# Kernel optimization log

Measured on AMD Instinct MI355X. Metric: run time of the kernel, lower is better.

The kernel has to match this reference:

```python
import jax, jax.numpy as jnp
import numpy as np

B, S, D, H, O = 4, 128, 768, 768, 2

def setup_inputs() -> dict:
    key = jax.random.key(0)
    ks = jax.random.split(key, 6)
    scale = 1.0 / np.sqrt(2 * D)
    return {
        "a": jax.random.normal(ks[0], (B, S, D), jnp.float32),
        "b": jax.random.normal(ks[1], (B, S, D), jnp.float32),
        "W1": jax.random.normal(ks[2], (2 * D, H), jnp.float32) * scale,
        "b1": jax.random.normal(ks[3], (H,), jnp.float32) * 0.01,
        "W2": jax.random.normal(ks[4], (H, O), jnp.float32) * (1.0 / np.sqrt(H)),
        "b2": jax.random.normal(ks[5], (O,), jnp.float32) * 0.01,
    }

def reference(a, b, W1, b1, W2, b2):
    # Pairwise concat [a_i ; b_j] followed by Linear(2D->H) is algebraically
    # identical to projecting a and b separately and broadcast-adding
    # (biaffine-style rewrite; same math as cat+matmul, less HBM traffic).
    d = a.shape[-1]
    ha = jnp.einsum('bsd,dh->bsh', a, W1[:d])        # (B, Sa, H)
    hb = jnp.einsum('btd,dh->bth', b, W1[d:])        # (B, Sb, H)
    h = jax.nn.relu(ha[:, :, None, :] + hb[:, None, :, :] + b1)  # (B, Sa, Sb, H)
    scores = jnp.einsum('bsth,ho->bsto', h, W2) + b2  # (B, Sa, Sb, O)
    return scores
```

## Files before the change

### kernel.cpp

```cpp
#include <hip/hip_runtime.h>
#include <hip/hip_fp16.h>


typedef __attribute__((ext_vector_type(2))) _Float16 half2t;
typedef __attribute__((ext_vector_type(8))) _Float16 half8t;
typedef __attribute__((ext_vector_type(4))) float floatx4;
typedef unsigned int uint;

__device__ __forceinline__ half2t pkrtz(float x, float y) {
    __fp16 r __attribute__((ext_vector_type(2))) = __builtin_amdgcn_cvt_pkrtz(x, y);
    half2t o; __builtin_memcpy(&o, &r, 4); return o;
}

__global__ __launch_bounds__(256) void gemm_kernel(
    const float* __restrict__ a, const float* __restrict__ bmat,
    const float* __restrict__ W1, const float* __restrict__ b1,
    const float* __restrict__ W2,
    ushort* __restrict__ Hf,
    uint* __restrict__ W2pk)
{
    const int which = blockIdx.z;
    const int n0 = blockIdx.x * 32;
    const int m0 = blockIdx.y * 32;
    const int t  = threadIdx.x;

    if (blockIdx.x == 0 && blockIdx.y == 0 && which == 0) {
#pragma unroll
        for (int j = t; j < 768; j += 256) {
            const int o  = (j >= 384) ? 1 : 0;
            const int h2 = j - o * 384;
            half2t pw = pkrtz(W2[4 * h2 + o], W2[4 * h2 + 2 + o]);
            uint u; __builtin_memcpy(&u, &pw, 4);
            W2pk[j] = u;
        }
    }

    __shared__ ushort As[2][32][72];
    __shared__ ushort Bs[2][32][72];

    const int arow = t >> 3;
    const int akc  = (t & 7) * 8;
    const float* __restrict__ Asrc = which ? bmat : a;
    const float* __restrict__ aptr = Asrc + (size_t)(m0 + arow) * 768 + akc;

    const int ncol = t & 31;
    const int kg   = (t >> 5) * 8;
    const float* __restrict__ bptr = W1 + (size_t)(which * 768 + kg) * 768 + n0 + ncol;

    const int lane = t & 63;
    const int w    = t >> 6;
    const int mh   = w >> 1;
    const int nh   = w & 1;
    const int lr   = lane & 15;
    const int lq   = lane >> 4;

    floatx4 acc = {0, 0, 0, 0};

    float4 a4[2];
    float  br[8];
    a4[0] = *(const float4*)(aptr);
    a4[1] = *(const float4*)(aptr + 4);
#pragma unroll
    for (int j = 0; j < 8; j++) br[j] = bptr[(size_t)j * 768];

    int p = 0;
    for (int kt = 0; kt < 768; kt += 64, p ^= 1) {
        half2t ap[4];
        ap[0] = pkrtz(a4[0].x, a4[0].y);
        ap[1] = pkrtz(a4[0].z, a4[0].w);
        ap[2] = pkrtz(a4[1].x, a4[1].y);
        ap[3] = pkrtz(a4[1].z, a4[1].w);
        __builtin_memcpy(&As[p][arow][akc], ap, 16);
        half2t bp[4];
#pragma unroll
        for (int j = 0; j < 4; j++) bp[j] = pkrtz(br[2 * j], br[2 * j + 1]);
        __builtin_memcpy(&Bs[p][ncol][kg], bp, 16);

        __syncthreads();

        if (kt + 64 < 768) {
            a4[0] = *(const float4*)(aptr + kt + 64);
            a4[1] = *(const float4*)(aptr + kt + 68);
#pragma unroll
            for (int j = 0; j < 8; j++)
                br[j] = bptr[(size_t)(kt + 64 + j) * 768];
        }

#pragma unroll
        for (int h = 0; h < 2; h++) {
            const int kb = h * 32 + lq * 8;
            half8t afr, bfr;
            __builtin_memcpy(&afr, &As[p][mh * 16 + lr][kb], 16);
            __builtin_memcpy(&bfr, &Bs[p][nh * 16 + lr][kb], 16);
            acc = __builtin_amdgcn_mfma_f32_16x16x32_f16(afr, bfr, acc, 0, 0, 0);
        }
    }

    const int ncolO = n0 + nh * 16 + lr;
    const float bias = which ? 0.f : b1[ncolO];
    ushort* __restrict__ dst = Hf + (size_t)which * 393216 + ncolO;
    const int rbase = m0 + mh * 16 + lq * 4;
#pragma unroll
    for (int r = 0; r < 4; r++) {
        _Float16 v = (_Float16)(acc[r] + bias);
        ushort u; __builtin_memcpy(&u, &v, 2);
        dst[(size_t)(rbase + r) * 768] = u;
    }
}

__global__ __launch_bounds__(256) void pair_kernel(
    const ushort* __restrict__ Hf, const uint* __restrict__ W2pk,
    const float* __restrict__ b2, float* __restrict__ out)
{
    const int bb = blockIdx.z >> 1;
    const int hh = blockIdx.z & 1;
    const int s0 = blockIdx.y * 16;
    const int t0 = blockIdx.x * 16;
    const int tid = threadIdx.x;

    __shared__ ushort hAs[16][392];
    __shared__ ushort hBs[16][392];

    const int hbase = hh * 384;
    const ushort* __restrict__ Asrc = Hf +          (size_t)(bb * 128 + s0) * 768 + hbase;
    const ushort* __restrict__ Bsrc = Hf + 393216 + (size_t)(bb * 128 + t0) * 768 + hbase;

#pragma unroll
    for (int i = 0; i < 3; i++) {
        const int c   = tid + i * 256;
        const int row = c / 48;
        const int col = (c % 48) * 8;
        *(uint4*)&hAs[row][col] = *(const uint4*)(Asrc + (size_t)row * 768 + col);
        *(uint4*)&hBs[row][col] = *(const uint4*)(Bsrc + (size_t)row * 768 + col);
    }
    __syncthreads();

    const int sl = tid >> 4;
    const int tl = tid & 15;
    const ushort* __restrict__ arow = &hAs[sl][0];
    const ushort* __restrict__ brow = &hBs[tl][0];
    const uint* __restrict__ w2o0 = W2pk +       hh * 192;
    const uint* __restrict__ w2o1 = W2pk + 384 + hh * 192;

    float acc0 = 0.f, acc1 = 0.f;
    const half2t zero = {(_Float16)0.f, (_Float16)0.f};

#pragma unroll 8
    for (int h8 = 0; h8 < 384; h8 += 8) {
        half2t pa[4], pb[4], w0[4], w1[4];
        __builtin_memcpy(pa, arow + h8, 16);
        __builtin_memcpy(pb, brow + h8, 16);
        __builtin_memcpy(w0, &w2o0[h8 / 2], 16);
        __builtin_memcpy(w1, &w2o1[h8 / 2], 16);
#pragma unroll
        for (int j = 0; j < 4; j++) {
            half2t s = pa[j] + pb[j];
            s = __builtin_elementwise_max(s, zero);
            acc0 = __builtin_amdgcn_fdot2(s, w0[j], acc0, false);
            acc1 = __builtin_amdgcn_fdot2(s, w1[j], acc1, false);
        }
    }

    if (hh == 0) { acc0 += b2[0]; acc1 += b2[1]; }
    const int sg = bb * 128 + s0 + sl;
    const int tg = t0 + tl;
    float* ob = &out[((size_t)sg * 128 + tg) * 2];
    unsafeAtomicAdd(ob,     acc0);
    unsafeAtomicAdd(ob + 1, acc1);
}

extern "C" void kernel_launch(void* const* d_in, const int* in_sizes, int n_in,
                              void* d_out, int out_size, void* d_ws, size_t ws_size,
                              hipStream_t stream) {
    const float* a  = (const float*)d_in[0];
    const float* b  = (const float*)d_in[1];
    const float* W1 = (const float*)d_in[2];
    const float* b1 = (const float*)d_in[3];
    const float* W2 = (const float*)d_in[4];
    const float* b2 = (const float*)d_in[5];
    float* out = (float*)d_out;

    ushort* Hf   = (ushort*)d_ws;
    uint*   W2pk = (uint*)((char*)d_ws + (2 << 20));

    gemm_kernel<<<dim3(24, 16, 2), 256, 0, stream>>>(a, b, W1, b1, W2, Hf, W2pk);
    pair_kernel<<<dim3(8, 8, 8), 256, 0, stream>>>(Hf, W2pk, b2, out);
}
```

Baseline: 85.15 us.

## Register-block pair kernel 2x2 per thread and split hidden dim eight ways

Each pair_kernel thread now computes a 2x2 block of (s,t) pairs, so every loaded A row, B row and W2 value is reused across four pairs and LDS and register load traffic per output drops. The hidden dimension is split into eight 96-wide slices instead of two 384-wide halves, which keeps the grid at 512 blocks while each block covers a 32x32 tile. The cost is four times as many atomic adds into the output and more accumulator registers per thread.

```diff
diff --git a/kernel.cpp b/kernel.cpp
--- a/kernel.cpp
+++ b/kernel.cpp
@@ -10,6 +10,9 @@
 __device__ __forceinline__ half2t pkrtz(float x, float y) {
     __fp16 r __attribute__((ext_vector_type(2))) = __builtin_amdgcn_cvt_pkrtz(x, y);
     half2t o; __builtin_memcpy(&o, &r, 4); return o;
+}
+__device__ __forceinline__ half2t h2cast(uint u) {
+    half2t o; __builtin_memcpy(&o, &u, 4); return o;
 }
 
 __global__ __launch_bounds__(256) void gemm_kernel(
@@ -112,61 +115,90 @@
     const ushort* __restrict__ Hf, const uint* __restrict__ W2pk,
     const float* __restrict__ b2, float* __restrict__ out)
 {
-    const int bb = blockIdx.z >> 1;
-    const int hh = blockIdx.z & 1;
-    const int s0 = blockIdx.y * 16;
-    const int t0 = blockIdx.x * 16;
+    const int bb = blockIdx.z >> 3;
+    const int hh = blockIdx.z & 7;
+    const int s0 = blockIdx.y * 32;
+    const int t0 = blockIdx.x * 32;
     const int tid = threadIdx.x;
 
-    __shared__ ushort hAs[16][392];
-    __shared__ ushort hBs[16][392];
-
-    const int hbase = hh * 384;
+    __shared__ ushort hAs[32][104];
+    __shared__ ushort hBs[32][104];
+
+    const int hbase = hh * 96;
     const ushort* __restrict__ Asrc = Hf +          (size_t)(bb * 128 + s0) * 768 + hbase;
     const ushort* __restrict__ Bsrc = Hf + 393216 + (size_t)(bb * 128 + t0) * 768 + hbase;
 
 #pragma unroll
     for (int i = 0; i < 3; i++) {
         const int c   = tid + i * 256;
-        const int row = c / 48;
-        const int col = (c % 48) * 8;
-        *(uint4*)&hAs[row][col] = *(const uint4*)(Asrc + (size_t)row * 768 + col);
-        *(uint4*)&hBs[row][col] = *(const uint4*)(Bsrc + (size_t)row * 768 + col);
+        const int arr = c >= 384;
+        const int cc  = c - arr * 384;
+        const int row = cc / 12;
+        const int ch  = (cc % 12) * 8;
+        const ushort* src = arr ? Bsrc : Asrc;
+        ushort* dst = arr ? &hBs[row][ch] : &hAs[row][ch];
+        *(uint4*)dst = *(const uint4*)(src + (size_t)row * 768 + ch);
     }
     __syncthreads();
 
     const int sl = tid >> 4;
     const int tl = tid & 15;
-    const ushort* __restrict__ arow = &hAs[sl][0];
-    const ushort* __restrict__ brow = &hBs[tl][0];
-    const uint* __restrict__ w2o0 = W2pk +       hh * 192;
-    const uint* __restrict__ w2o1 = W2pk + 384 + hh * 192;
-
-    float acc0 = 0.f, acc1 = 0.f;
+    const ushort* __restrict__ arow0 = &hAs[2 * sl][0];
+    const ushort* __restrict__ arow1 = &hAs[2 * sl + 1][0];
+    const ushort* __restrict__ brow0 = &hBs[2 * tl][0];
+    const ushort* __restrict__ brow1 = &hBs[2 * tl + 1][0];
+    const uint* __restrict__ w2o0 = W2pk +       hh * 48;
+    const uint* __restrict__ w2o1 = W2pk + 384 + hh * 48;
+
+    float acc[2][2][2] = {};
     const half2t zero = {(_Float16)0.f, (_Float16)0.f};
 
-#pragma unroll 8
-    for (int h8 = 0; h8 < 384; h8 += 8) {
-        half2t pa[4], pb[4], w0[4], w1[4];
-        __builtin_memcpy(pa, arow + h8, 16);
-        __builtin_memcpy(pb, brow + h8, 16);
+#pragma unroll
+    for (int h8 = 0; h8 < 96; h8 += 8) {
+        uint pa0[4], pa1[4], pb0[4], pb1[4], w0[4], w1[4];
+        __builtin_memcpy(pa0, arow0 + h8, 16);
+        __builtin_memcpy(pa1, arow1 + h8, 16);
+        __builtin_memcpy(pb0, brow0 + h8, 16);
+        __builtin_memcpy(pb1, brow1 + h8, 16);
         __builtin_memcpy(w0, &w2o0[h8 / 2], 16);
         __builtin_memcpy(w1, &w2o1[h8 / 2], 16);
 #pragma unroll
-        for (int j = 0; j < 4; j++) {
-            half2t s = pa[j] + pb[j];
-            s = __builtin_elementwise_max(s, zero);
-            acc0 = __builtin_amdgcn_fdot2(s, w0[j], acc0, false);
-            acc1 = __builtin_amdgcn_fdot2(s, w1[j], acc1, false);
-        }
-    }
-
-    if (hh == 0) { acc0 += b2[0]; acc1 += b2[1]; }
-    const int sg = bb * 128 + s0 + sl;
-    const int tg = t0 + tl;
-    float* ob = &out[((size_t)sg * 128 + tg) * 2];
-    unsafeAtomicAdd(ob,     acc0);
-    unsafeAtomicAdd(ob + 1, acc1);
+        for (int d = 0; d < 4; d++) {
+            const half2t a0 = h2cast(pa0[d]), a1 = h2cast(pa1[d]);
+            const half2t b0 = h2cast(pb0[d]), b1 = h2cast(pb1[d]);
+            const half2t v0 = h2cast(w0[d]),  v1 = h2cast(w1[d]);
+            half2t s;
+            s = __builtin_elementwise_max(a0 + b0, zero);
+            acc[0][0][0] = __builtin_amdgcn_fdot2(s, v0, acc[0][0][0], false);
+            acc[0][0][1] = __builtin_amdgcn_fdot2(s, v1, acc[0][0][1], false);
+            s = __builtin_elementwise_max(a0 + b1, zero);
+            acc[0][1][0] = __builtin_amdgcn_fdot2(s, v0, acc[0][1][0], false);
+            acc[0][1][1] = __builtin_amdgcn_fdot2(s, v1, acc[0][1][1], false);
+            s = __builtin_elementwise_max(a1 + b0, zero);
+            acc[1][0][0] = __builtin_amdgcn_fdot2(s, v0, acc[1][0][0], false);
+            acc[1][0][1] = __builtin_amdgcn_fdot2(s, v1, acc[1][0][1], false);
+            s = __builtin_elementwise_max(a1 + b1, zero);
+            acc[1][1][0] = __builtin_amdgcn_fdot2(s, v0, acc[1][1][0], false);
+            acc[1][1][1] = __builtin_amdgcn_fdot2(s, v1, acc[1][1][1], false);
+        }
+    }
+
+    if (hh == 0) {
+#pragma unroll
+        for (int i = 0; i < 2; i++)
+#pragma unroll
+            for (int j = 0; j < 2; j++) {
+                acc[i][j][0] += b2[0];
+                acc[i][j][1] += b2[1];
+            }
+    }
+    const int sg = bb * 128 + s0 + 2 * sl;
+    const int tg = t0 + 2 * tl;
+    float* ob = &out[(size_t)sg * 256 + tg * 2];
+    unsafeAtomicAdd(ob + 0,   acc[0][0][0]); unsafeAtomicAdd(ob + 1,   acc[0][0][1]);
+    unsafeAtomicAdd(ob + 2,   acc[0][1][0]); unsafeAtomicAdd(ob + 3,   acc[0][1][1]);
+    unsafeAtomicAdd(ob + 256, acc[1][0][0]); unsafeAtomicAdd(ob + 257, acc[1][0][1]);
+    unsafeAtomicAdd(ob + 258, acc[1][1][0]); unsafeAtomicAdd(ob + 259, acc[1][1][1]);
 }
 
 extern "C" void kernel_launch(void* const* d_in, const int* in_sizes, int n_in,
@@ -184,5 +216,5 @@
     uint*   W2pk = (uint*)((char*)d_ws + (2 << 20));
 
     gemm_kernel<<<dim3(24, 16, 2), 256, 0, stream>>>(a, b, W1, b1, W2, Hf, W2pk);
-    pair_kernel<<<dim3(8, 8, 8), 256, 0, stream>>>(Hf, W2pk, b2, out);
-}
+    pair_kernel<<<dim3(4, 4, 32), 256, 0, stream>>>(Hf, W2pk, b2, out);
+}
```

Result: slower. 93.27 us (+9.5%).
